# Kernel tuning notes

Hardware: AMD Instinct MI355X
Metric: run time of the kernel (lower is better)

The kernel has to match this reference:

```python
import jax, jax.numpy as jnp
import numpy as np


def setup_inputs() -> dict:
    key = jax.random.key(0)
    k1, k2, k3, k4 = jax.random.split(key, 4)
    B, C, H, W = 4, 256, 64, 64
    Va = jax.random.normal(k1, (B, C, H, W), jnp.float32)
    Vb = jax.random.normal(k2, (B, C, H, W), jnp.float32)
    # nn.Linear(C, C, bias=False) weight, used as x @ W^T
    W_linear = jax.random.normal(k3, (C, C), jnp.float32) * 0.05
    # nn.Conv2d(C, 1, 1, bias=False) weight, init normal_(0, 0.01)
    W_gate = jax.random.normal(k4, (C,), jnp.float32) * 0.01
    return {"Va_output": Va, "Vb_output": Vb, "W_linear": W_linear,
            "W_gate": W_gate, "input_size": 512}


def reference(Va_output, Vb_output, W_linear, W_gate, input_size):
    B, C, H, W = Vb_output.shape
    A = H * W  # all_dim
    Va_flat = Va_output.reshape(B, C, A)  # [B, C, A]
    Vb_flat = Vb_output.reshape(B, C, A)
    # linear on transposed A-major tokens: Va_t @ W_linear^T -> [B, A, C]
    Va_corr = jnp.einsum('bca,dc->bad', Va_flat, W_linear)
    # correlation matrix S = Va_corr @ Vb_flat -> [B, A, A]
    S = jnp.einsum('bac,can->ban'[:3] + 'c,c' if False else 'bac,cn', Va_corr, Vb_flat) if False else jnp.einsum('bac,bcn->ban', Va_corr, Vb_flat)
    # S_c = softmax(S, dim=1); S_r = softmax(S^T, dim=1) = softmax(S, axis=2)^T
    S_c = jax.nn.softmax(S, axis=1)
    S_r = jnp.swapaxes(jax.nn.softmax(S, axis=2), 1, 2)
    Vb_att = jnp.einsum('bca,ban->bcn', Va_flat, S_r).reshape(B, C, H, W)
    Va_att = jnp.einsum('bca,ban->bcn', Vb_flat, S_c).reshape(B, C, H, W)
    # 1x1 gate conv (C -> 1, no bias) + sigmoid
    Va_mask = jax.nn.sigmoid(jnp.einsum('bchw,c->bhw', Va_att, W_gate))[:, None]
    Vb_mask = jax.nn.sigmoid(jnp.einsum('bchw,c->bhw', Vb_att, W_gate))[:, None]
    Va_out = jnp.concatenate([Va_att * Va_mask, Va_output], axis=1)  # [B, 2C, H, W]
    Vb_out = jnp.concatenate([Vb_att * Vb_mask, Vb_output], axis=1)
    return (Va_out, Vb_out, input_size)
```

## Files before the change

kernel.cpp:

```cpp
#include <hip/hip_runtime.h>

typedef _Float16 f16;
typedef f16 f16x8 __attribute__((ext_vector_type(8)));
typedef float f32x4 __attribute__((ext_vector_type(4)));
typedef short b16x8 __attribute__((ext_vector_type(8)));
typedef unsigned short u16;
typedef u16 u16x4 __attribute__((ext_vector_type(4)));

#define MFMA_F16(a,b,c)  __builtin_amdgcn_mfma_f32_16x16x32_f16((a),(b),(c),0,0,0)
#define MFMA_BF16(a,b,c) __builtin_amdgcn_mfma_f32_16x16x32_bf16((a),(b),(c),0,0,0)

static __device__ __forceinline__ u16 bf16rn(float f) {
    unsigned u = __builtin_bit_cast(unsigned, f);
    u += 0x7FFFu + ((u >> 16) & 1u);
    return (u16)(u >> 16);
}

typedef const __attribute__((address_space(1))) unsigned int* gas_p;
typedef __attribute__((address_space(3))) unsigned int* las_p;
static __device__ __forceinline__ void gll16(const void* g, void* l) {
    __builtin_amdgcn_global_load_lds((gas_p)g, (las_p)l, 16, 0, 0);
}

static constexpr int B_ = 4, C_ = 256, A_ = 4096;
static constexpr int CA   = C_ * A_;
static constexpr int BCA  = B_ * CA;
static constexpr int OUT_T = B_ * 2 * CA;
static constexpr size_t WS_Va16 = 0;
static constexpr size_t WS_Vb16 = WS_Va16 + (size_t)BCA;
static constexpr size_t WS_VaT  = WS_Vb16 + (size_t)BCA;
static constexpr size_t WS_VbT  = WS_VaT  + (size_t)BCA;
static constexpr size_t WS_Q1   = WS_VbT  + (size_t)BCA;
static constexpr size_t WS_W16  = WS_Q1   + (size_t)BCA;
static constexpr size_t WS_HALFS = WS_W16 + (size_t)(C_ * C_);

static constexpr float M0 = 48.0f;

__global__ void coatt_convw(const float* __restrict__ W, f16* __restrict__ W16) {
    int i = blockIdx.x * 256 + threadIdx.x;
    W16[i] = (f16)W[i];
}

__global__ void coatt_transpose(const float* __restrict__ Va,
                                const float* __restrict__ Vb,
                                u16* __restrict__ ws) {
    __shared__ f16 tile[64][73];
    int z = blockIdx.z; int b = z >> 1; int which = z & 1;
    const float* src = which ? Vb : Va;
    char* vt = (char*)(ws + (which ? WS_Vb16 : WS_Va16)) + (size_t)b * CA * 2;
    char* kt = (char*)(ws + (which ? WS_VbT : WS_VaT)) + (size_t)b * CA * 2;
    int a0 = blockIdx.x * 64, c0 = blockIdx.y * 64;
    int t = threadIdx.x;
    int r = t >> 2, q = t & 3;

    const float* sp = src + (size_t)(b * C_ + c0 + r) * A_ + a0 + q * 16;
    f16 h[16] __attribute__((aligned(16)));
    u16 hb[16] __attribute__((aligned(16)));
#pragma unroll
    for (int i = 0; i < 4; ++i) {
        float4 v = *(const float4*)(sp + i * 4);
        h[i*4+0] = (f16)v.x; h[i*4+1] = (f16)v.y;
        h[i*4+2] = (f16)v.z; h[i*4+3] = (f16)v.w;
        hb[i*4+0] = bf16rn(v.x); hb[i*4+1] = bf16rn(v.y);
        hb[i*4+2] = bf16rn(v.z); hb[i*4+3] = bf16rn(v.w);
    }
    char* vb8 = vt + (size_t)(a0 >> 6) * 32768 + (c0 + r) * 16;
    *(u16x4*)(vb8 + (q * 2 + 0) * 4096 + 0) = *(const u16x4*)&hb[0];
    *(u16x4*)(vb8 + (q * 2 + 0) * 4096 + 8) = *(const u16x4*)&hb[4];
    *(u16x4*)(vb8 + (q * 2 + 1) * 4096 + 0) = *(const u16x4*)&hb[8];
    *(u16x4*)(vb8 + (q * 2 + 1) * 4096 + 8) = *(const u16x4*)&hb[12];
#pragma unroll
    for (int i = 0; i < 16; ++i) tile[r][q * 16 + i] = h[i];
    __syncthreads();
    f16 ht[16] __attribute__((aligned(16)));
#pragma unroll
    for (int i = 0; i < 16; ++i) ht[i] = tile[q * 16 + i][r];
    char* kb8 = kt + (size_t)(a0 >> 6) * 32768 + r * 16;
    *(f16x8*)(kb8 + (size_t)(c0 / 8 + q * 2 + 0) * 1024) = *(const f16x8*)&ht[0];
    *(f16x8*)(kb8 + (size_t)(c0 / 8 + q * 2 + 1) * 1024) = *(const f16x8*)&ht[8];
}

__global__ __launch_bounds__(256) void coatt_q1(const u16* __restrict__ ws_) {
    const char* vat = (const char*)(ws_ + WS_VaT);
    const f16* w16 = (const f16*)(ws_ + WS_W16);
    char* q1 = (char*)(ws_ + WS_Q1);
    int b = blockIdx.y; int a0 = blockIdx.x * 64;
    int tid = threadIdx.x, wave = tid >> 6, lane = tid & 63;
    int m = lane & 15, quad = lane >> 4;

    const char* Ab = vat + (size_t)b * CA * 2 + (size_t)(a0 >> 6) * 32768;
    f16x8 af[8];
#pragma unroll
    for (int kc = 0; kc < 8; ++kc)
        af[kc] = *(const f16x8*)(Ab + (kc * 4 + quad) * 1024 + (wave * 16 + m) * 16);

    f32x4 acc[16];
#pragma unroll
    for (int t = 0; t < 16; ++t) acc[t] = (f32x4){0.f, 0.f, 0.f, 0.f};

#pragma unroll
    for (int kc = 0; kc < 8; ++kc) {
#pragma unroll
        for (int t = 0; t < 16; ++t) {
            f16x8 bf = *(const f16x8*)(w16 + (size_t)(t * 16 + m) * C_ + kc * 32 + quad * 8);
            acc[t] = MFMA_F16(af[kc], bf, acc[t]);
        }
    }
    char* Qb = q1 + (size_t)b * CA * 2 + (size_t)(a0 >> 6) * 32768;
#pragma unroll
    for (int t = 0; t < 16; ++t) {
#pragma unroll
        for (int r = 0; r < 4; ++r) {
            int al = wave * 16 + quad * 4 + r;
            int d = t * 16 + m;
            f16 v = (f16)acc[t][r];
            *(u16*)(Qb + (size_t)(d >> 3) * 1024 + al * 16 + (d & 7) * 2) =
                __builtin_bit_cast(u16, v);
        }
    }
}

__global__ __launch_bounds__(512, 2) void coatt_flash(const u16* __restrict__ ws,
                                                      const float* __restrict__ Wgate,
                                                      float* __restrict__ dout) {
    __shared__ __align__(16) char smem[153600];
    char* Plds = smem + 131072;
    float* Lsum = (float*)(smem + 149504);
    float* Gsum = (float*)(smem + 151552);
    float* Olds = (float*)smem;

    int p = blockIdx.x;
    int vc = p & 7;
    int b = vc & 3, att = vc >> 2;
    int n0 = (p >> 3) * 128;

    const char *Qp, *Kp, *Vp; float* outp;
    const char* base = (const char*)ws;
    size_t boff = (size_t)b * CA * 2;
    if (att == 0) {
        Qp = base + WS_Q1 * 2 + boff;
        Kp = base + WS_VbT * 2 + boff;
        Vp = base + WS_Va16 * 2 + boff;
        outp = dout + (size_t)OUT_T + (size_t)b * 2 * CA;
    } else {
        Qp = base + WS_VbT * 2 + boff;
        Kp = base + WS_Q1 * 2 + boff;
        Vp = base + WS_Vb16 * 2 + boff;
        outp = dout + (size_t)b * 2 * CA;
    }

    int tid = threadIdx.x, wave = tid >> 6, lane = tid & 63;
    int iq = wave >> 2, jq = wave & 3;
    int m = lane & 15, quad = lane >> 4;

    f16x8 qf[4][8];
    {
        const char* qb = Qp + (size_t)((n0 >> 6) + iq) * 32768;
#pragma unroll
        for (int qt = 0; qt < 4; ++qt)
#pragma unroll
            for (int kc = 0; kc < 8; ++kc)
                qf[qt][kc] = *(const f16x8*)(qb + (kc * 4 + quad) * 1024 +
                                             (qt * 16 + m) * 16);
    }

    f32x4 Oacc[4][4];
#pragma unroll
    for (int qt = 0; qt < 4; ++qt)
#pragma unroll
        for (int ct = 0; ct < 4; ++ct) Oacc[qt][ct] = (f32x4){0.f, 0.f, 0.f, 0.f};
    float lpart[4] = {0.f, 0.f, 0.f, 0.f};

    const char* ksrc = Kp + wave * 1024 + lane * 16;
    const char* vsrc = Vp + wave * 1024 + lane * 16;

    {
#pragma unroll
        for (int ii = 0; ii < 4; ++ii)
            gll16(ksrc + ii * 8192, smem + wave * 1024 + ii * 8192);
#pragma unroll
        for (int ii = 0; ii < 4; ++ii)
            gll16(vsrc + ii * 8192, smem + 65536 + wave * 1024 + ii * 8192);
    }

    for (int kb = 0; kb < 64; ++kb) {
        int cur = kb & 1, nxt = cur ^ 1;
        char* Kc = smem + cur * 32768;
        char* Vc = smem + 65536 + cur * 32768;
        __syncthreads();

        if (kb < 63) {
            const char* kg = ksrc + (size_t)(kb + 1) * 32768;
            char* kl = smem + nxt * 32768 + wave * 1024;
#pragma unroll
            for (int ii = 0; ii < 4; ++ii) gll16(kg + ii * 8192, kl + ii * 8192);
        }

        f32x4 Sc[4];
#pragma unroll
        for (int qt = 0; qt < 4; ++qt) Sc[qt] = (f32x4){0.f, 0.f, 0.f, 0.f};
#pragma unroll
        for (int kc = 0; kc < 8; ++kc) {
            f16x8 kf = *(const f16x8*)(Kc + (kc * 4 + quad) * 1024 +
                                       (jq * 16 + m) * 16);
#pragma unroll
            for (int qt = 0; qt < 4; ++qt)
                Sc[qt] = MFMA_F16(kf, qf[qt][kc], Sc[qt]);
        }

#pragma unroll
        for (int qt = 0; qt < 4; ++qt) {
            int q = iq * 64 + qt * 16 + m;
            u16x4 pk;
            float s4 = 0.f;
#pragma unroll
            for (int r = 0; r < 4; ++r) {
                float pv = __expf(Sc[qt][r] - M0);
                s4 += pv;
                pk[r] = bf16rn(pv);
            }
            lpart[qt] += s4;
            *(u16x4*)(Plds + q * 144 + jq * 32 + quad * 8) = pk;
        }
        __syncthreads();

        if (kb < 63) {
            const char* vg = vsrc + (size_t)(kb + 1) * 32768;
            char* vl = smem + 65536 + nxt * 32768 + wave * 1024;
#pragma unroll
            for (int ii = 0; ii < 4; ++ii) gll16(vg + ii * 8192, vl + ii * 8192);
        }

#pragma unroll
        for (int s = 0; s < 2; ++s) {
            b16x8 pf[4];
#pragma unroll
            for (int qt = 0; qt < 4; ++qt) {
                int q = iq * 64 + qt * 16 + m;
                pf[qt] = *(const b16x8*)(Plds + q * 144 + s * 64 + quad * 16);
            }
#pragma unroll
            for (int ct = 0; ct < 4; ++ct) {
                int c = jq * 64 + ct * 16 + m;
                b16x8 vf = *(const b16x8*)(Vc + (s * 4 + quad) * 4096 + c * 16);
#pragma unroll
                for (int qt = 0; qt < 4; ++qt)
                    Oacc[qt][ct] = MFMA_BF16(pf[qt], vf, Oacc[qt][ct]);
            }
        }
    }

#pragma unroll
    for (int qt = 0; qt < 4; ++qt) {
        float v = lpart[qt];
        v += __shfl_xor(v, 16);
        v += __shfl_xor(v, 32);
        lpart[qt] = v;
    }
    __syncthreads();
    if (lane < 16) {
#pragma unroll
        for (int qt = 0; qt < 4; ++qt)
            Lsum[wave * 64 + qt * 16 + lane] = lpart[qt];
    }
    __syncthreads();
    float inv[4][4];
#pragma unroll
    for (int qt = 0; qt < 4; ++qt)
#pragma unroll
        for (int r = 0; r < 4; ++r) {
            int ql = qt * 16 + quad * 4 + r;
            float s = Lsum[(iq * 4 + 0) * 64 + ql] + Lsum[(iq * 4 + 1) * 64 + ql] +
                      Lsum[(iq * 4 + 2) * 64 + ql] + Lsum[(iq * 4 + 3) * 64 + ql];
            inv[qt][r] = 1.0f / s;
        }
    float gp[4][4] = {{0,0,0,0},{0,0,0,0},{0,0,0,0},{0,0,0,0}};
#pragma unroll
    for (int ct = 0; ct < 4; ++ct) {
        float w = Wgate[jq * 64 + ct * 16 + m];
#pragma unroll
        for (int qt = 0; qt < 4; ++qt)
#pragma unroll
            for (int r = 0; r < 4; ++r) {
                float o = Oacc[qt][ct][r] * inv[qt][r];
                Oacc[qt][ct][r] = o;
                gp[qt][r] += o * w;
            }
    }
#pragma unroll
    for (int qt = 0; qt < 4; ++qt)
#pragma unroll
        for (int r = 0; r < 4; ++r) {
            float v = gp[qt][r];
            v += __shfl_xor(v, 1); v += __shfl_xor(v, 2);
            v += __shfl_xor(v, 4); v += __shfl_xor(v, 8);
            gp[qt][r] = v;
        }
    if (m == 0) {
#pragma unroll
        for (int qt = 0; qt < 4; ++qt)
#pragma unroll
            for (int r = 0; r < 4; ++r)
                Gsum[wave * 64 + qt * 16 + quad * 4 + r] = gp[qt][r];
    }
    __syncthreads();
#pragma unroll
    for (int qt = 0; qt < 4; ++qt)
#pragma unroll
        for (int r = 0; r < 4; ++r) {
            int ql = qt * 16 + quad * 4 + r;
            float g = Gsum[(iq * 4 + 0) * 64 + ql] + Gsum[(iq * 4 + 1) * 64 + ql] +
                      Gsum[(iq * 4 + 2) * 64 + ql] + Gsum[(iq * 4 + 3) * 64 + ql];
            float msk = 1.0f / (1.0f + __expf(-g));
#pragma unroll
            for (int ct = 0; ct < 4; ++ct) Oacc[qt][ct][r] *= msk;
        }

    for (int hf = 0; hf < 2; ++hf) {
        __syncthreads();
        if ((jq >> 1) == hf) {
#pragma unroll
            for (int ct = 0; ct < 4; ++ct)
#pragma unroll
                for (int qt = 0; qt < 4; ++qt) {
                    int cl = (jq & 1) * 64 + ct * 16 + m;
                    float4 v;
                    v.x = Oacc[qt][ct][0]; v.y = Oacc[qt][ct][1];
                    v.z = Oacc[qt][ct][2]; v.w = Oacc[qt][ct][3];
                    *(float4*)(Olds + cl * 132 + iq * 64 + qt * 16 + quad * 4) = v;
                }
        }
        __syncthreads();
#pragma unroll
        for (int ii = 0; ii < 8; ++ii) {
            int ci = tid + ii * 512;
            int c = ci >> 5, ch = (ci & 31) * 4;
            float4 v = *(const float4*)(Olds + c * 132 + ch);
            *(float4*)(outp + (size_t)(hf * 128 + c) * A_ + n0 + ch) = v;
        }
    }
}

__global__ void coatt_copy(const float* __restrict__ Va, const float* __restrict__ Vb,
                           const int* __restrict__ psz, float* __restrict__ dout) {
    int base = blockIdx.x * 256 + threadIdx.x;
    const float4* va4 = (const float4*)Va;
    const float4* vb4 = (const float4*)Vb;
    float4* out4 = (float4*)dout;
#pragma unroll
    for (int i = 0; i < 4; ++i) {
        int idx = base + i * 524288;
        int t = idx >> 20;
        int r = idx & 1048575;
        int b = r >> 18;
        int rr = r & 262143;
        float4 v = t ? vb4[r] : va4[r];
        out4[(size_t)t * 2097152 + (size_t)b * 524288 + 262144 + rr] = v;
    }
    if (base == 0) dout[16777216] = (float)(*psz);
}

extern "C" void kernel_launch(void* const* d_in, const int* in_sizes, int n_in,
                              void* d_out, int out_size, void* d_ws, size_t ws_size,
                              hipStream_t stream) {
    const float* Va = (const float*)d_in[0];
    const float* Vb = (const float*)d_in[1];
    const float* Wl = (const float*)d_in[2];
    const float* Wg = (const float*)d_in[3];
    const int* psz  = (const int*)d_in[4];
    float* out = (float*)d_out;
    u16* ws = (u16*)d_ws;

    if (ws_size < WS_HALFS * sizeof(u16)) return;

    coatt_convw<<<256, 256, 0, stream>>>(Wl, (f16*)(ws + WS_W16));
    coatt_transpose<<<dim3(64, 4, 8), 256, 0, stream>>>(Va, Vb, ws);
    coatt_q1<<<dim3(64, 4), 256, 0, stream>>>(ws);
    coatt_flash<<<256, 512, 0, stream>>>(ws, Wg, out);
    coatt_copy<<<2048, 256, 0, stream>>>(Va, Vb, psz, out);
}
```

Measured before the change: 268.1 us.

## Software-pipeline QK and PV stages with double-buffered swizzled P tile

Restructures the flash loop so the PV MFMAs for the previous key block run in the same iteration as the QK MFMAs and exp for the current block. P is double-buffered in LDS with an XOR swizzle instead of a padded stride, and the V prefetch moves to the start of the iteration. This cuts the loop from two barriers to one and lets QK and PV work interleave. In exchange LDS use grows to 160 KB, which may limit occupancy to one block per CU despite launch_bounds(512,2), and the Lsum/Gsum buffers now alias the P region.

Measured after the change: 258.1 us. 3.7% less time.

```diff
diff --git a/kernel.cpp b/kernel.cpp
--- a/kernel.cpp
+++ b/kernel.cpp
@@ -123,10 +123,10 @@
 __global__ __launch_bounds__(512, 2) void coatt_flash(const u16* __restrict__ ws,
                                                       const float* __restrict__ Wgate,
                                                       float* __restrict__ dout) {
-    __shared__ __align__(16) char smem[153600];
+    __shared__ __align__(16) char smem[163840];
     char* Plds = smem + 131072;
-    float* Lsum = (float*)(smem + 149504);
-    float* Gsum = (float*)(smem + 151552);
+    float* Lsum = (float*)(smem + 131072);
+    float* Gsum = (float*)(smem + 131072 + 2048);
     float* Olds = (float*)smem;
 
     int p = blockIdx.x;
@@ -174,26 +174,32 @@
     const char* ksrc = Kp + wave * 1024 + lane * 16;
     const char* vsrc = Vp + wave * 1024 + lane * 16;
 
-    {
-#pragma unroll
-        for (int ii = 0; ii < 4; ++ii)
-            gll16(ksrc + ii * 8192, smem + wave * 1024 + ii * 8192);
-#pragma unroll
-        for (int ii = 0; ii < 4; ++ii)
-            gll16(vsrc + ii * 8192, smem + 65536 + wave * 1024 + ii * 8192);
-    }
+    int pswz = m & 7;
+    int pw_off = ((jq * 2 + (quad >> 1)) ^ pswz) * 16 + (quad & 1) * 8;
+    int pr_off0 = ((0 * 4 + quad) ^ pswz) * 16;
+    int pr_off1 = ((1 * 4 + quad) ^ pswz) * 16;
+
+#pragma unroll
+    for (int ii = 0; ii < 4; ++ii)
+        gll16(ksrc + ii * 8192, smem + wave * 1024 + ii * 8192);
+    __syncthreads();
 
     for (int kb = 0; kb < 64; ++kb) {
         int cur = kb & 1, nxt = cur ^ 1;
         char* Kc = smem + cur * 32768;
-        char* Vc = smem + 65536 + cur * 32768;
-        __syncthreads();
+        char* Pw = Plds + cur * 16384;
 
         if (kb < 63) {
             const char* kg = ksrc + (size_t)(kb + 1) * 32768;
             char* kl = smem + nxt * 32768 + wave * 1024;
 #pragma unroll
             for (int ii = 0; ii < 4; ++ii) gll16(kg + ii * 8192, kl + ii * 8192);
+        }
+        {
+            const char* vg = vsrc + (size_t)kb * 32768;
+            char* vl = smem + 65536 + cur * 32768 + wave * 1024;
+#pragma unroll
+            for (int ii = 0; ii < 4; ++ii) gll16(vg + ii * 8192, vl + ii * 8192);
         }
 
         f32x4 Sc[4];
@@ -220,29 +226,51 @@
                 pk[r] = bf16rn(pv);
             }
             lpart[qt] += s4;
-            *(u16x4*)(Plds + q * 144 + jq * 32 + quad * 8) = pk;
-        }
+            *(u16x4*)(Pw + q * 128 + pw_off) = pk;
+        }
+
+        if (kb > 0) {
+            char* Pr = Plds + nxt * 16384;
+            char* Vr = smem + 65536 + nxt * 32768;
+#pragma unroll
+            for (int s = 0; s < 2; ++s) {
+                int pro = s ? pr_off1 : pr_off0;
+                b16x8 pf[4];
+#pragma unroll
+                for (int qt = 0; qt < 4; ++qt) {
+                    int q = iq * 64 + qt * 16 + m;
+                    pf[qt] = *(const b16x8*)(Pr + q * 128 + pro);
+                }
+#pragma unroll
+                for (int ct = 0; ct < 4; ++ct) {
+                    int c = jq * 64 + ct * 16 + m;
+                    b16x8 vf = *(const b16x8*)(Vr + (s * 4 + quad) * 4096 + c * 16);
+#pragma unroll
+                    for (int qt = 0; qt < 4; ++qt)
+                        Oacc[qt][ct] = MFMA_BF16(pf[qt], vf, Oacc[qt][ct]);
+                }
+            }
+        }
+
         __syncthreads();
-
-        if (kb < 63) {
-            const char* vg = vsrc + (size_t)(kb + 1) * 32768;
-            char* vl = smem + 65536 + nxt * 32768 + wave * 1024;
-#pragma unroll
-            for (int ii = 0; ii < 4; ++ii) gll16(vg + ii * 8192, vl + ii * 8192);
-        }
-
+    }
+
+    {
+        char* Pr = Plds + 16384;
+        char* Vr = smem + 65536 + 32768;
 #pragma unroll
         for (int s = 0; s < 2; ++s) {
+            int pro = s ? pr_off1 : pr_off0;
             b16x8 pf[4];
 #pragma unroll
             for (int qt = 0; qt < 4; ++qt) {
                 int q = iq * 64 + qt * 16 + m;
-                pf[qt] = *(const b16x8*)(Plds + q * 144 + s * 64 + quad * 16);
+                pf[qt] = *(const b16x8*)(Pr + q * 128 + pro);
             }
 #pragma unroll
             for (int ct = 0; ct < 4; ++ct) {
                 int c = jq * 64 + ct * 16 + m;
-                b16x8 vf = *(const b16x8*)(Vc + (s * 4 + quad) * 4096 + c * 16);
+                b16x8 vf = *(const b16x8*)(Vr + (s * 4 + quad) * 4096 + c * 16);
 #pragma unroll
                 for (int qt = 0; qt < 4; ++qt)
                     Oacc[qt][ct] = MFMA_BF16(pf[qt], vf, Oacc[qt][ct]);
```
